# Kernel optimization log

Measured on AMD Instinct MI355X. Metric: run time of the kernel, lower is better.

Reference implementation:

```python
import jax, jax.numpy as jnp
import numpy as np


def _project(feat, x, y):
    """Bilinear sample feat [H,W,C] at float coords (x along H, y along W) -> [N,C]."""
    H, W, _ = feat.shape
    x1 = jnp.floor(x)
    x2 = jnp.minimum(jnp.ceil(x), H - 1.0)
    y1 = jnp.floor(y)
    y2 = jnp.minimum(jnp.ceil(y), W - 1.0)
    xi1, xi2 = x1.astype(jnp.int32), x2.astype(jnp.int32)
    yi1, yi2 = y1.astype(jnp.int32), y2.astype(jnp.int32)
    Q11 = feat[xi1, yi1]  # [N,C]
    Q12 = feat[xi1, yi2]
    Q21 = feat[xi2, yi1]
    Q22 = feat[xi2, yi2]
    w11 = ((x2 - x) * (y2 - y))[:, None]
    w21 = ((x - x1) * (y2 - y))[:, None]
    w12 = ((x2 - x) * (y - y1))[:, None]
    w22 = ((x - x1) * (y - y1))[:, None]
    return w11 * Q11 + w21 * Q21 + w12 * Q12 + w22 * Q22


def setup_inputs() -> dict:
    key = jax.random.key(0)
    k0, k1, k2, k3, k4, k5 = jax.random.split(key, 6)
    N = 100000
    xy = jax.random.normal(k0, (N, 2), dtype=jnp.float32) * 0.5
    # Z must be strictly negative for the perspective division by -Z
    z = -(jax.random.uniform(k5, (N, 1), dtype=jnp.float32) * 2.0 + 0.5)
    coords = jnp.concatenate([xy, z], axis=1)
    feat1 = jax.random.normal(k1, (56, 56, 64), dtype=jnp.float32)
    feat2 = jax.random.normal(k2, (28, 28, 128), dtype=jnp.float32)
    feat3 = jax.random.normal(k3, (14, 14, 256), dtype=jnp.float32)
    feat4 = jax.random.normal(k4, (7, 7, 512), dtype=jnp.float32)
    return {"coords": coords, "feat1": feat1, "feat2": feat2,
            "feat3": feat3, "feat4": feat4}


def reference(coords, feat1, feat2, feat3, feat4):
    X = coords[:, 0]
    Y = coords[:, 1]
    Z = coords[:, 2]
    h = 250.0 * (-Y) / (-Z) + 112.0
    w = 250.0 * X / (-Z) + 112.0
    h = jnp.clip(h, 0.0, 223.0)
    w = jnp.clip(w, 0.0, 223.0)
    outs = [coords]
    for feat, size in ((feat1, 56.0), (feat2, 28.0), (feat3, 14.0), (feat4, 7.0)):
        x = h / (224.0 / size)
        y = w / (224.0 / size)
        outs.append(_project(feat, x, y))
    return jnp.concatenate(outs, axis=1)  # [N, 3+64+128+256+512]
```

## Files before the change

kernel.cpp:

```cpp
#include <hip/hip_runtime.h>


#define PTS  4
#define ROWF 963
#define GPP  240

typedef float fx4 __attribute__((ext_vector_type(4)));

__global__ __launch_bounds__(256) void graphproj_kernel(
    const float* __restrict__ coords,
    const float* __restrict__ f1, const float* __restrict__ f2,
    const float* __restrict__ f3, const float* __restrict__ f4,
    float* __restrict__ out, int N)
{
    __shared__ __align__(16) float smem[PTS * ROWF];
    __shared__ __align__(16) float s_w[PTS][4][4];
    __shared__ const float* s_q[PTS][4][4];

    const int b  = blockIdx.x;
    const int t  = threadIdx.x;
    const int p0 = b * PTS;
    const int npts = min(PTS, N - p0);

    if (t < 4 * npts) {
        const int pt = t >> 2;
        const int lv = t & 3;
        const int p  = p0 + pt;
        const float X = coords[p * 3 + 0];
        const float Y = coords[p * 3 + 1];
        const float Z = coords[p * 3 + 2];
        float h = 250.0f * (-Y) / (-Z) + 112.0f;
        float w = 250.0f * X / (-Z) + 112.0f;
        h = fminf(fmaxf(h, 0.0f), 223.0f);
        w = fminf(fmaxf(w, 0.0f), 223.0f);

        const int   Hs[4] = {56, 28, 14, 7};
        const int   Cs[4] = {64, 128, 256, 512};
        const int   H = Hs[lv], C = Cs[lv];
        const float scale = (float)H / 224.0f;
        const float x = h * scale, y = w * scale;
        const float x1f = floorf(x), x2f = fminf(ceilf(x), (float)(H - 1));
        const float y1f = floorf(y), y2f = fminf(ceilf(y), (float)(H - 1));
        const int xi1 = (int)x1f, xi2 = (int)x2f;
        const int yi1 = (int)y1f, yi2 = (int)y2f;

        s_w[pt][lv][0] = (x2f - x) * (y2f - y);
        s_w[pt][lv][1] = (x - x1f) * (y2f - y);
        s_w[pt][lv][2] = (x2f - x) * (y - y1f);
        s_w[pt][lv][3] = (x - x1f) * (y - y1f);

        const float* f = (lv == 0) ? f1 : (lv == 1) ? f2 : (lv == 2) ? f3 : f4;
        s_q[pt][lv][0] = f + (size_t)(xi1 * H + yi1) * C;
        s_q[pt][lv][1] = f + (size_t)(xi2 * H + yi1) * C;
        s_q[pt][lv][2] = f + (size_t)(xi1 * H + yi2) * C;
        s_q[pt][lv][3] = f + (size_t)(xi2 * H + yi2) * C;
    }
    if (t >= 64 && t < 64 + 3 * npts) {
        const int i = t - 64;
        smem[(i / 3) * ROWF + (i % 3)] = coords[p0 * 3 + i];
    }
    __syncthreads();

    for (int gf = t; gf < npts * GPP; gf += 256) {
        const int pt = gf / GPP;
        const int g  = gf - pt * GPP;
        const int lv = (g >= 16) + (g >= 48) + (g >= 112);
        const int c4 = g - ((lv == 0) ? 0 : (lv == 1) ? 16 : (lv == 2) ? 48 : 112);

        const float4 wv = *(const float4*)&s_w[pt][lv][0];
        const fx4* q11 = (const fx4*)s_q[pt][lv][0];
        const fx4* q21 = (const fx4*)s_q[pt][lv][1];
        const fx4* q12 = (const fx4*)s_q[pt][lv][2];
        const fx4* q22 = (const fx4*)s_q[pt][lv][3];

        const fx4 a  = q11[c4];
        const fx4 bb = q21[c4];
        const fx4 c  = q12[c4];
        const fx4 d  = q22[c4];

        float* o = &smem[pt * ROWF + 3 + 4 * g];
        o[0] = wv.x * a.x + wv.y * bb.x + wv.z * c.x + wv.w * d.x;
        o[1] = wv.x * a.y + wv.y * bb.y + wv.z * c.y + wv.w * d.y;
        o[2] = wv.x * a.z + wv.y * bb.z + wv.z * c.z + wv.w * d.z;
        o[3] = wv.x * a.w + wv.y * bb.w + wv.z * c.w + wv.w * d.w;
    }
    __syncthreads();

    if (npts == PTS) {
        const fx4* src = (const fx4*)smem;
        fx4* dst = (fx4*)(out + (size_t)p0 * ROWF);
        for (int i = t; i < PTS * ROWF / 4; i += 256) {
            __builtin_nontemporal_store(src[i], &dst[i]);
        }
    } else {
        for (int i = t; i < npts * ROWF; i += 256) {
            out[(size_t)p0 * ROWF + i] = smem[i];
        }
    }
}

extern "C" void kernel_launch(void* const* d_in, const int* in_sizes, int n_in,
                              void* d_out, int out_size, void* d_ws, size_t ws_size,
                              hipStream_t stream) {
    const float* coords = (const float*)d_in[0];
    const float* f1 = (const float*)d_in[1];
    const float* f2 = (const float*)d_in[2];
    const float* f3 = (const float*)d_in[3];
    const float* f4 = (const float*)d_in[4];
    float* out = (float*)d_out;
    const int N = in_sizes[0] / 3;

    const int blocks = (N + PTS - 1) / PTS;
    graphproj_kernel<<<blocks, 256, 0, stream>>>(coords, f1, f2, f3, f4, out, N);
}
```

Baseline: 80.14 us.

## Write bilinear results directly to global memory, skipping the shared-memory staging

Removes the shared-memory output buffer. Each thread now blends two float4 groups per iteration and writes them straight to global memory with unaligned nontemporal vector stores. The aim is to drop the LDS round trip, one barrier and a large LDS allocation, which should raise occupancy. In exchange, the 963-float row stride makes the global stores misaligned relative to 16 bytes, which may split or slow them, and the tail block now falls back to a scalar path.

```diff
diff --git a/kernel.cpp b/kernel.cpp
--- a/kernel.cpp
+++ b/kernel.cpp
@@ -3,9 +3,21 @@
 
 #define PTS  4
 #define ROWF 963
-#define GPP  240
+#define GP2  120
 
-typedef float fx4 __attribute__((ext_vector_type(4)));
+typedef float fx4  __attribute__((ext_vector_type(4)));
+typedef float fx4u __attribute__((ext_vector_type(4), aligned(4)));
+
+static __device__ __forceinline__ fx4 blend4(const float4 w,
+                                             const fx4 a, const fx4 b,
+                                             const fx4 c, const fx4 d) {
+    fx4 r;
+    r.x = w.x * a.x + w.y * b.x + w.z * c.x + w.w * d.x;
+    r.y = w.x * a.y + w.y * b.y + w.z * c.y + w.w * d.y;
+    r.z = w.x * a.z + w.y * b.z + w.z * c.z + w.w * d.z;
+    r.w = w.x * a.w + w.y * b.w + w.z * c.w + w.w * d.w;
+    return r;
+}
 
 __global__ __launch_bounds__(256) void graphproj_kernel(
     const float* __restrict__ coords,
@@ -13,7 +25,6 @@
     const float* __restrict__ f3, const float* __restrict__ f4,
     float* __restrict__ out, int N)
 {
-    __shared__ __align__(16) float smem[PTS * ROWF];
     __shared__ __align__(16) float s_w[PTS][4][4];
     __shared__ const float* s_q[PTS][4][4];
 
@@ -34,9 +45,8 @@
         h = fminf(fmaxf(h, 0.0f), 223.0f);
         w = fminf(fmaxf(w, 0.0f), 223.0f);
 
-        const int   Hs[4] = {56, 28, 14, 7};
-        const int   Cs[4] = {64, 128, 256, 512};
-        const int   H = Hs[lv], C = Cs[lv];
+        const int H = (lv == 0) ? 56 : (lv == 1) ? 28 : (lv == 2) ? 14 : 7;
+        const int C = (lv == 0) ? 64 : (lv == 1) ? 128 : (lv == 2) ? 256 : 512;
         const float scale = (float)H / 224.0f;
         const float x = h * scale, y = w * scale;
         const float x1f = floorf(x), x2f = fminf(ceilf(x), (float)(H - 1));
@@ -55,46 +65,53 @@
         s_q[pt][lv][2] = f + (size_t)(xi1 * H + yi2) * C;
         s_q[pt][lv][3] = f + (size_t)(xi2 * H + yi2) * C;
     }
-    if (t >= 64 && t < 64 + 3 * npts) {
+    if (npts == PTS && t >= 64 && t < 64 + 3 * PTS) {
         const int i = t - 64;
-        smem[(i / 3) * ROWF + (i % 3)] = coords[p0 * 3 + i];
-    }
-    __syncthreads();
-
-    for (int gf = t; gf < npts * GPP; gf += 256) {
-        const int pt = gf / GPP;
-        const int g  = gf - pt * GPP;
-        const int lv = (g >= 16) + (g >= 48) + (g >= 112);
-        const int c4 = g - ((lv == 0) ? 0 : (lv == 1) ? 16 : (lv == 2) ? 48 : 112);
-
-        const float4 wv = *(const float4*)&s_w[pt][lv][0];
-        const fx4* q11 = (const fx4*)s_q[pt][lv][0];
-        const fx4* q21 = (const fx4*)s_q[pt][lv][1];
-        const fx4* q12 = (const fx4*)s_q[pt][lv][2];
-        const fx4* q22 = (const fx4*)s_q[pt][lv][3];
-
-        const fx4 a  = q11[c4];
-        const fx4 bb = q21[c4];
-        const fx4 c  = q12[c4];
-        const fx4 d  = q22[c4];
-
-        float* o = &smem[pt * ROWF + 3 + 4 * g];
-        o[0] = wv.x * a.x + wv.y * bb.x + wv.z * c.x + wv.w * d.x;
-        o[1] = wv.x * a.y + wv.y * bb.y + wv.z * c.y + wv.w * d.y;
-        o[2] = wv.x * a.z + wv.y * bb.z + wv.z * c.z + wv.w * d.z;
-        o[3] = wv.x * a.w + wv.y * bb.w + wv.z * c.w + wv.w * d.w;
+        out[(size_t)(p0 + i / 3) * ROWF + (i % 3)] = coords[p0 * 3 + i];
     }
     __syncthreads();
 
     if (npts == PTS) {
-        const fx4* src = (const fx4*)smem;
-        fx4* dst = (fx4*)(out + (size_t)p0 * ROWF);
-        for (int i = t; i < PTS * ROWF / 4; i += 256) {
-            __builtin_nontemporal_store(src[i], &dst[i]);
+        for (int gf = t; gf < PTS * GP2; gf += 256) {
+            const int pt = gf / GP2;
+            const int g2 = gf - pt * GP2;
+            const int g  = g2 * 2;
+            const int lv = (g >= 16) + (g >= 48) + (g >= 112);
+            const int c4 = g - ((lv == 0) ? 0 : (lv == 1) ? 16 : (lv == 2) ? 48 : 112);
+
+            const float4 wv = *(const float4*)&s_w[pt][lv][0];
+            const fx4* q11 = (const fx4*)s_q[pt][lv][0];
+            const fx4* q21 = (const fx4*)s_q[pt][lv][1];
+            const fx4* q12 = (const fx4*)s_q[pt][lv][2];
+            const fx4* q22 = (const fx4*)s_q[pt][lv][3];
+
+            const fx4 a0 = q11[c4],     b0 = q21[c4],     c0 = q12[c4],     d0 = q22[c4];
+            const fx4 a1 = q11[c4 + 1], b1 = q21[c4 + 1], c1 = q12[c4 + 1], d1 = q22[c4 + 1];
+
+            const fx4 r0 = blend4(wv, a0, b0, c0, d0);
+            const fx4 r1 = blend4(wv, a1, b1, c1, d1);
+
+            float* o = out + (size_t)(p0 + pt) * ROWF + 3 + 4 * g;
+            __builtin_nontemporal_store(r0, (fx4u*)o);
+            __builtin_nontemporal_store(r1, (fx4u*)(o + 4));
         }
     } else {
         for (int i = t; i < npts * ROWF; i += 256) {
-            out[(size_t)p0 * ROWF + i] = smem[i];
+            const int pt = i / ROWF;
+            const int r  = i - pt * ROWF;
+            float v;
+            if (r < 3) {
+                v = coords[(p0 + pt) * 3 + r];
+            } else {
+                const int c  = r - 3;
+                const int lv = (c >= 64) + (c >= 192) + (c >= 448);
+                const int cc = c - ((lv == 0) ? 0 : (lv == 1) ? 64 : (lv == 2) ? 192 : 448);
+                v = s_w[pt][lv][0] * s_q[pt][lv][0][cc]
+                  + s_w[pt][lv][1] * s_q[pt][lv][1][cc]
+                  + s_w[pt][lv][2] * s_q[pt][lv][2][cc]
+                  + s_w[pt][lv][3] * s_q[pt][lv][3][cc];
+            }
+            out[(size_t)p0 * ROWF + i] = v;
         }
     }
 }
```

After: 90.31 us. 12.7% more time.

## Write bilinear outputs directly to global memory instead of staging in LDS

Applied to the files above, without the earlier changes.

Removes the shared-memory row staging buffer and the second barrier, computing one output float per thread and storing it directly to global memory with scalar loads of the four corner features. The goal is to save LDS traffic and a sync. It gives up the aligned float4 nontemporal stores and vectorized feature loads, so it may issue more memory instructions and lose the streaming-store cache hint.

```diff
diff --git a/kernel.cpp b/kernel.cpp
--- a/kernel.cpp
+++ b/kernel.cpp
@@ -3,9 +3,6 @@
 
 #define PTS  4
 #define ROWF 963
-#define GPP  240
-
-typedef float fx4 __attribute__((ext_vector_type(4)));
 
 __global__ __launch_bounds__(256) void graphproj_kernel(
     const float* __restrict__ coords,
@@ -13,8 +10,7 @@
     const float* __restrict__ f3, const float* __restrict__ f4,
     float* __restrict__ out, int N)
 {
-    __shared__ __align__(16) float smem[PTS * ROWF];
-    __shared__ __align__(16) float s_w[PTS][4][4];
+    __shared__ float s_w[PTS][4][4];
     __shared__ const float* s_q[PTS][4][4];
 
     const int b  = blockIdx.x;
@@ -34,9 +30,8 @@
         h = fminf(fmaxf(h, 0.0f), 223.0f);
         w = fminf(fmaxf(w, 0.0f), 223.0f);
 
-        const int   Hs[4] = {56, 28, 14, 7};
-        const int   Cs[4] = {64, 128, 256, 512};
-        const int   H = Hs[lv], C = Cs[lv];
+        const int H = (lv == 0) ? 56 : (lv == 1) ? 28 : (lv == 2) ? 14 : 7;
+        const int C = (lv == 0) ? 64 : (lv == 1) ? 128 : (lv == 2) ? 256 : 512;
         const float scale = (float)H / 224.0f;
         const float x = h * scale, y = w * scale;
         const float x1f = floorf(x), x2f = fminf(ceilf(x), (float)(H - 1));
@@ -57,44 +52,36 @@
     }
     if (t >= 64 && t < 64 + 3 * npts) {
         const int i = t - 64;
-        smem[(i / 3) * ROWF + (i % 3)] = coords[p0 * 3 + i];
+        out[(size_t)(p0 + i / 3) * ROWF + (i % 3)] = coords[p0 * 3 + i];
     }
     __syncthreads();
 
-    for (int gf = t; gf < npts * GPP; gf += 256) {
-        const int pt = gf / GPP;
-        const int g  = gf - pt * GPP;
-        const int lv = (g >= 16) + (g >= 48) + (g >= 112);
-        const int c4 = g - ((lv == 0) ? 0 : (lv == 1) ? 16 : (lv == 2) ? 48 : 112);
-
-        const float4 wv = *(const float4*)&s_w[pt][lv][0];
-        const fx4* q11 = (const fx4*)s_q[pt][lv][0];
-        const fx4* q21 = (const fx4*)s_q[pt][lv][1];
-        const fx4* q12 = (const fx4*)s_q[pt][lv][2];
-        const fx4* q22 = (const fx4*)s_q[pt][lv][3];
-
-        const fx4 a  = q11[c4];
-        const fx4 bb = q21[c4];
-        const fx4 c  = q12[c4];
-        const fx4 d  = q22[c4];
-
-        float* o = &smem[pt * ROWF + 3 + 4 * g];
-        o[0] = wv.x * a.x + wv.y * bb.x + wv.z * c.x + wv.w * d.x;
-        o[1] = wv.x * a.y + wv.y * bb.y + wv.z * c.y + wv.w * d.y;
-        o[2] = wv.x * a.z + wv.y * bb.z + wv.z * c.z + wv.w * d.z;
-        o[3] = wv.x * a.w + wv.y * bb.w + wv.z * c.w + wv.w * d.w;
-    }
-    __syncthreads();
-
-    if (npts == PTS) {
-        const fx4* src = (const fx4*)smem;
-        fx4* dst = (fx4*)(out + (size_t)p0 * ROWF);
-        for (int i = t; i < PTS * ROWF / 4; i += 256) {
-            __builtin_nontemporal_store(src[i], &dst[i]);
+    const int total = npts * 960;
+    if (total == PTS * 960) {
+        #pragma unroll 3
+        for (int k = 0; k < PTS * 960 / 256; ++k) {
+            const int f  = t + 256 * k;
+            const int pt = f / 960;
+            const int c  = f - pt * 960;
+            const int lv = (c >= 64) + (c >= 192) + (c >= 448);
+            const int cc = c - ((lv == 0) ? 0 : (lv == 1) ? 64 : (lv == 2) ? 192 : 448);
+            const float v = s_w[pt][lv][0] * s_q[pt][lv][0][cc]
+                          + s_w[pt][lv][1] * s_q[pt][lv][1][cc]
+                          + s_w[pt][lv][2] * s_q[pt][lv][2][cc]
+                          + s_w[pt][lv][3] * s_q[pt][lv][3][cc];
+            out[(size_t)p0 * ROWF + (size_t)pt * ROWF + 3 + c] = v;
         }
     } else {
-        for (int i = t; i < npts * ROWF; i += 256) {
-            out[(size_t)p0 * ROWF + i] = smem[i];
+        for (int f = t; f < total; f += 256) {
+            const int pt = f / 960;
+            const int c  = f - pt * 960;
+            const int lv = (c >= 64) + (c >= 192) + (c >= 448);
+            const int cc = c - ((lv == 0) ? 0 : (lv == 1) ? 64 : (lv == 2) ? 192 : 448);
+            const float v = s_w[pt][lv][0] * s_q[pt][lv][0][cc]
+                          + s_w[pt][lv][1] * s_q[pt][lv][1][cc]
+                          + s_w[pt][lv][2] * s_q[pt][lv][2][cc]
+                          + s_w[pt][lv][3] * s_q[pt][lv][3][cc];
+            out[(size_t)p0 * ROWF + (size_t)pt * ROWF + 3 + c] = v;
         }
     }
 }
```

After: 151.2 us. 88.7% more time.

## Swizzle shared staging buffer to avoid bank conflicts; store int offsets instead of pointers

Applied to the files above, without the earlier changes.

Results are written into the shared staging row with a per-16-byte-group element rotation, then un-rotated in registers before the nontemporal vector store to global. Each row starts at a misaligned offset of 3 floats, so the scalar shared writes and the float4 reads conflicted; the rotation is meant to spread those accesses across banks. Feature-row pointers are replaced by 32-bit offsets loaded as one int4, and the tail block now computes its outputs directly from global memory. The extra index arithmetic and vector shuffles add ALU work to a kernel that is mostly memory-bound.

```diff
diff --git a/kernel.cpp b/kernel.cpp
--- a/kernel.cpp
+++ b/kernel.cpp
@@ -7,6 +7,14 @@
 
 typedef float fx4 __attribute__((ext_vector_type(4)));
 
+__device__ __forceinline__ int rot_of(int g) { return (g + (g >> 3)) & 3; }
+
+__device__ __forceinline__ void store1(float* smem, int a, float v) {
+    const int g = a >> 2;
+    const int e = ((a & 3) + g + (g >> 3)) & 3;
+    smem[(g << 2) | e] = v;
+}
+
 __global__ __launch_bounds__(256) void graphproj_kernel(
     const float* __restrict__ coords,
     const float* __restrict__ f1, const float* __restrict__ f2,
@@ -15,7 +23,7 @@
 {
     __shared__ __align__(16) float smem[PTS * ROWF];
     __shared__ __align__(16) float s_w[PTS][4][4];
-    __shared__ const float* s_q[PTS][4][4];
+    __shared__ __align__(16) int   s_off[PTS][4][4];
 
     const int b  = blockIdx.x;
     const int t  = threadIdx.x;
@@ -34,9 +42,8 @@
         h = fminf(fmaxf(h, 0.0f), 223.0f);
         w = fminf(fmaxf(w, 0.0f), 223.0f);
 
-        const int   Hs[4] = {56, 28, 14, 7};
-        const int   Cs[4] = {64, 128, 256, 512};
-        const int   H = Hs[lv], C = Cs[lv];
+        const int H = (lv == 0) ? 56 : (lv == 1) ? 28 : (lv == 2) ? 14 : 7;
+        const int C = (lv == 0) ? 64 : (lv == 1) ? 128 : (lv == 2) ? 256 : 512;
         const float scale = (float)H / 224.0f;
         const float x = h * scale, y = w * scale;
         const float x1f = floorf(x), x2f = fminf(ceilf(x), (float)(H - 1));
@@ -49,52 +56,74 @@
         s_w[pt][lv][2] = (x2f - x) * (y - y1f);
         s_w[pt][lv][3] = (x - x1f) * (y - y1f);
 
-        const float* f = (lv == 0) ? f1 : (lv == 1) ? f2 : (lv == 2) ? f3 : f4;
-        s_q[pt][lv][0] = f + (size_t)(xi1 * H + yi1) * C;
-        s_q[pt][lv][1] = f + (size_t)(xi2 * H + yi1) * C;
-        s_q[pt][lv][2] = f + (size_t)(xi1 * H + yi2) * C;
-        s_q[pt][lv][3] = f + (size_t)(xi2 * H + yi2) * C;
+        s_off[pt][lv][0] = (xi1 * H + yi1) * C;
+        s_off[pt][lv][1] = (xi2 * H + yi1) * C;
+        s_off[pt][lv][2] = (xi1 * H + yi2) * C;
+        s_off[pt][lv][3] = (xi2 * H + yi2) * C;
     }
     if (t >= 64 && t < 64 + 3 * npts) {
         const int i = t - 64;
-        smem[(i / 3) * ROWF + (i % 3)] = coords[p0 * 3 + i];
-    }
-    __syncthreads();
-
-    for (int gf = t; gf < npts * GPP; gf += 256) {
-        const int pt = gf / GPP;
-        const int g  = gf - pt * GPP;
-        const int lv = (g >= 16) + (g >= 48) + (g >= 112);
-        const int c4 = g - ((lv == 0) ? 0 : (lv == 1) ? 16 : (lv == 2) ? 48 : 112);
-
-        const float4 wv = *(const float4*)&s_w[pt][lv][0];
-        const fx4* q11 = (const fx4*)s_q[pt][lv][0];
-        const fx4* q21 = (const fx4*)s_q[pt][lv][1];
-        const fx4* q12 = (const fx4*)s_q[pt][lv][2];
-        const fx4* q22 = (const fx4*)s_q[pt][lv][3];
-
-        const fx4 a  = q11[c4];
-        const fx4 bb = q21[c4];
-        const fx4 c  = q12[c4];
-        const fx4 d  = q22[c4];
-
-        float* o = &smem[pt * ROWF + 3 + 4 * g];
-        o[0] = wv.x * a.x + wv.y * bb.x + wv.z * c.x + wv.w * d.x;
-        o[1] = wv.x * a.y + wv.y * bb.y + wv.z * c.y + wv.w * d.y;
-        o[2] = wv.x * a.z + wv.y * bb.z + wv.z * c.z + wv.w * d.z;
-        o[3] = wv.x * a.w + wv.y * bb.w + wv.z * c.w + wv.w * d.w;
+        store1(smem, (i / 3) * ROWF + (i % 3), coords[p0 * 3 + i]);
     }
     __syncthreads();
 
     if (npts == PTS) {
-        const fx4* src = (const fx4*)smem;
-        fx4* dst = (fx4*)(out + (size_t)p0 * ROWF);
-        for (int i = t; i < PTS * ROWF / 4; i += 256) {
-            __builtin_nontemporal_store(src[i], &dst[i]);
+        for (int gf = t; gf < PTS * GPP; gf += 256) {
+            const int pt = gf / GPP;
+            const int g  = gf - pt * GPP;
+            const int lv = (g >= 16) + (g >= 48) + (g >= 112);
+            const int c4 = g - ((lv == 0) ? 0 : (lv == 1) ? 16 : (lv == 2) ? 48 : 112);
+
+            const float4 wv = *(const float4*)&s_w[pt][lv][0];
+            const int4   ov = *(const int4*)&s_off[pt][lv][0];
+            const float* base = (lv == 0) ? f1 : (lv == 1) ? f2 : (lv == 2) ? f3 : f4;
+
+            const fx4 a  = ((const fx4*)(base + ov.x))[c4];
+            const fx4 bb = ((const fx4*)(base + ov.y))[c4];
+            const fx4 c  = ((const fx4*)(base + ov.z))[c4];
+            const fx4 d  = ((const fx4*)(base + ov.w))[c4];
+
+            fx4 r;
+            r.x = wv.x * a.x + wv.y * bb.x + wv.z * c.x + wv.w * d.x;
+            r.y = wv.x * a.y + wv.y * bb.y + wv.z * c.y + wv.w * d.y;
+            r.z = wv.x * a.z + wv.y * bb.z + wv.z * c.z + wv.w * d.z;
+            r.w = wv.x * a.w + wv.y * bb.w + wv.z * c.w + wv.w * d.w;
+
+            const int L = pt * ROWF + 3 + 4 * g;
+            store1(smem, L + 0, r.x);
+            store1(smem, L + 1, r.y);
+            store1(smem, L + 2, r.z);
+            store1(smem, L + 3, r.w);
+        }
+        __syncthreads();
+
+        const fx4* sp  = (const fx4*)smem;
+        fx4*       dst = (fx4*)(out + (size_t)p0 * ROWF);
+        for (int j = t; j < PTS * ROWF / 4; j += 256) {
+            const fx4 v = sp[j];
+            const int r = rot_of(j);
+            const fx4 t2 = (r & 2) ? (fx4){v.z, v.w, v.x, v.y} : v;
+            const fx4 u  = (r & 1) ? (fx4){t2.y, t2.z, t2.w, t2.x} : t2;
+            __builtin_nontemporal_store(u, &dst[j]);
         }
     } else {
         for (int i = t; i < npts * ROWF; i += 256) {
-            out[(size_t)p0 * ROWF + i] = smem[i];
+            const int pt = i / ROWF;
+            const int rr = i - pt * ROWF;
+            float v;
+            if (rr < 3) {
+                v = coords[(p0 + pt) * 3 + rr];
+            } else {
+                const int c  = rr - 3;
+                const int lv = (c >= 64) + (c >= 192) + (c >= 448);
+                const int cc = c - ((lv == 0) ? 0 : (lv == 1) ? 64 : (lv == 2) ? 192 : 448);
+                const float* base = (lv == 0) ? f1 : (lv == 1) ? f2 : (lv == 2) ? f3 : f4;
+                v = s_w[pt][lv][0] * base[s_off[pt][lv][0] + cc]
+                  + s_w[pt][lv][1] * base[s_off[pt][lv][1] + cc]
+                  + s_w[pt][lv][2] * base[s_off[pt][lv][2] + cc]
+                  + s_w[pt][lv][3] * base[s_off[pt][lv][3] + cc];
+            }
+            out[(size_t)p0 * ROWF + i] = v;
         }
     }
 }
```

Measured after the change: 86.31 us. 1.08x slower.
